# Kernel optimization log

Measured on AMD Instinct MI355X. Metric: run time of the kernel, lower is better.

Reference implementation:

```python
import jax, jax.numpy as jnp
import numpy as np

DELTA = 0.1
PAD = 2  # kernel_size // 2


def _step(x, W):
    # circular padding then VALID 5x5 cross-correlation (matches torch Conv2d circular)
    xp = jnp.pad(x, ((0, 0), (0, 0), (PAD, PAD), (PAD, PAD)), mode='wrap')
    y = jax.lax.conv_general_dilated(
        xp, W, window_strides=(1, 1), padding='VALID',
        dimension_numbers=('NCHW', 'OIHW', 'NCHW'))
    return jnp.clip(x + DELTA * jax.nn.relu(y), 0.0, 1.0)


def setup_inputs() -> dict:
    key = jax.random.key(0)
    k1, k2 = jax.random.split(key)
    x = jax.random.uniform(k1, (16, 3, 1024, 1024), dtype=jnp.float32)
    W = jax.random.normal(k2, (3, 3, 5, 5), dtype=jnp.float32) * 0.2
    return {"x": x, "W": W, "steps": 10}


def reference(x, W, steps):
    for _ in range(steps):
        x = _step(x, W)
    return x
```

## Files before the change

kernel.cpp:

```cpp
#include <hip/hip_runtime.h>


#define HH 1024
#define WW 1024
#define CC 3
#define NB 16
#define KR 2
#define TW 128
#define TH 8
#define LW (TW + 2*KR)
#define LH (TH + 2*KR)
#define DELTA 0.1f

__global__ __launch_bounds__(256)
void ca_step(const float* __restrict__ src, float* __restrict__ dst,
             const float* __restrict__ Wg) {
    __shared__ float tile[CC][LH][LW];
    __shared__ float wsm[CC * 5 * 16];

    const int tid = threadIdx.x;
    const int w0 = blockIdx.x * TW;
    const int h0 = blockIdx.y * TH;
    const int n  = blockIdx.z;

    if (tid < CC * CC * 25) {
        int oc = tid / 75;
        int rem = tid - oc * 75;
        int ic = rem / 25;
        int r2 = rem - ic * 25;
        int kh = r2 / 5;
        int kw = r2 - kh * 5;
        wsm[(ic * 5 + kh) * 16 + oc * 5 + kw] = Wg[tid];
    }

    const float* srcn = src + (size_t)n * CC * HH * WW;
    for (int idx = tid; idx < CC * LH * LW; idx += 256) {
        int c   = idx / (LH * LW);
        int rem = idx - c * (LH * LW);
        int r   = rem / LW;
        int col = rem - r * LW;
        int gh = (h0 + r - KR) & (HH - 1);
        int gw = (w0 + col - KR) & (WW - 1);
        tile[c][r][col] = srcn[((size_t)c * HH + gh) * WW + gw];
    }
    __syncthreads();

    const int tx = tid & 31;
    const int ty = tid >> 5;
    const int xb = tx * 4;

    float acc[CC][4];
#pragma unroll
    for (int oc = 0; oc < CC; ++oc)
#pragma unroll
        for (int j = 0; j < 4; ++j) acc[oc][j] = 0.f;

#pragma unroll
    for (int ic = 0; ic < CC; ++ic) {
#pragma unroll
        for (int kh = 0; kh < 5; ++kh) {
            const float* trow = &tile[ic][ty + kh][xb];
            float v[8];
#pragma unroll
            for (int t = 0; t < 8; ++t) v[t] = trow[t];
            const float* wrow = &wsm[(ic * 5 + kh) * 16];
#pragma unroll
            for (int oc = 0; oc < CC; ++oc) {
#pragma unroll
                for (int kw = 0; kw < 5; ++kw) {
                    const float wv = wrow[oc * 5 + kw];
#pragma unroll
                    for (int j = 0; j < 4; ++j)
                        acc[oc][j] = fmaf(v[kw + j], wv, acc[oc][j]);
                }
            }
        }
    }

    float* dstn = dst + (size_t)n * CC * HH * WW;
    const int h = h0 + ty;
#pragma unroll
    for (int oc = 0; oc < CC; ++oc) {
        float4 o;
        float r0 = fmaxf(acc[oc][0], 0.f);
        float r1 = fmaxf(acc[oc][1], 0.f);
        float r2 = fmaxf(acc[oc][2], 0.f);
        float r3 = fmaxf(acc[oc][3], 0.f);
        o.x = fminf(fmaxf(tile[oc][ty + KR][xb + KR + 0] + DELTA * r0, 0.f), 1.f);
        o.y = fminf(fmaxf(tile[oc][ty + KR][xb + KR + 1] + DELTA * r1, 0.f), 1.f);
        o.z = fminf(fmaxf(tile[oc][ty + KR][xb + KR + 2] + DELTA * r2, 0.f), 1.f);
        o.w = fminf(fmaxf(tile[oc][ty + KR][xb + KR + 3] + DELTA * r3, 0.f), 1.f);
        *(float4*)&dstn[((size_t)oc * HH + h) * WW + w0 + xb] = o;
    }
}

extern "C" void kernel_launch(void* const* d_in, const int* in_sizes, int n_in,
                              void* d_out, int out_size, void* d_ws, size_t ws_size,
                              hipStream_t stream) {
    (void)in_sizes; (void)n_in; (void)out_size;
    const float* x  = (const float*)d_in[0];
    const float* Wg = (const float*)d_in[1];
    const int STEPS = 10;
    float* out = (float*)d_out;
    const size_t buf_bytes = (size_t)NB * CC * HH * WW * sizeof(float);

    dim3 grid(WW / TW, HH / TH, NB);
    dim3 block(256);

    if (ws_size >= buf_bytes) {
        float* tmp = (float*)d_ws;
        const float* s = x;
        for (int i = 1; i <= STEPS; ++i) {
            float* d = (i & 1) ? tmp : out;
            ca_step<<<grid, block, 0, stream>>>(s, d, Wg);
            s = d;
        }
    } else {
        float* tmp = (float*)d_in[0];
        const float* s = x;
        for (int i = 1; i <= STEPS; ++i) {
            float* d = (i & 1) ? out : tmp;
            ca_step<<<grid, block, 0, stream>>>(s, d, Wg);
            s = d;
        }
        hipMemcpyAsync(out, tmp, buf_bytes, hipMemcpyDeviceToDevice, stream);
    }
}
```

Before: 1.740 ms.

## Double tile height, vectorize halo loads and shared reads, reuse weights across two rows

Measured after the change: 1.498 ms. 1.16x faster.

```diff
diff --git a/kernel.cpp b/kernel.cpp
--- a/kernel.cpp
+++ b/kernel.cpp
@@ -5,11 +5,10 @@
 #define WW 1024
 #define CC 3
 #define NB 16
-#define KR 2
 #define TW 128
-#define TH 8
-#define LW (TW + 2*KR)
-#define LH (TH + 2*KR)
+#define TH 16
+#define LW 132
+#define LH 20
 #define DELTA 0.1f
 
 __global__ __launch_bounds__(256)
@@ -22,6 +21,7 @@
     const int w0 = blockIdx.x * TW;
     const int h0 = blockIdx.y * TH;
     const int n  = blockIdx.z;
+    const float* srcn = src + (size_t)n * CC * HH * WW;
 
     if (tid < CC * CC * 25) {
         int oc = tid / 75;
@@ -33,64 +33,97 @@
         wsm[(ic * 5 + kh) * 16 + oc * 5 + kw] = Wg[tid];
     }
 
-    const float* srcn = src + (size_t)n * CC * HH * WW;
-    for (int idx = tid; idx < CC * LH * LW; idx += 256) {
-        int c   = idx / (LH * LW);
-        int rem = idx - c * (LH * LW);
-        int r   = rem / LW;
-        int col = rem - r * LW;
-        int gh = (h0 + r - KR) & (HH - 1);
-        int gw = (w0 + col - KR) & (WW - 1);
-        tile[c][r][col] = srcn[((size_t)c * HH + gh) * WW + gw];
+    for (int f = tid; f < CC * LH * 32; f += 256) {
+        int c   = f / (LH * 32);
+        int rem = f - c * (LH * 32);
+        int row = rem >> 5;
+        int c4  = rem & 31;
+        int gh = (h0 + row - 2) & (HH - 1);
+        const float4 v = *(const float4*)&srcn[((size_t)c * HH + gh) * WW + w0 + 4 * c4];
+        float* t = &tile[c][row][2 + 4 * c4];
+        *(float2*)&t[0] = make_float2(v.x, v.y);
+        *(float2*)&t[2] = make_float2(v.z, v.w);
+    }
+    if (tid < CC * LH * 2) {
+        int side = tid & 1;
+        int rf   = tid >> 1;
+        int c    = rf / LH;
+        int row  = rf - c * LH;
+        int gh = (h0 + row - 2) & (HH - 1);
+        int gw = side ? ((w0 + TW) & (WW - 1)) : ((w0 - 2) & (WW - 1));
+        const float2 v = *(const float2*)&srcn[((size_t)c * HH + gh) * WW + gw];
+        *(float2*)&tile[c][row][side ? (2 + TW) : 0] = v;
     }
     __syncthreads();
 
     const int tx = tid & 31;
     const int ty = tid >> 5;
-    const int xb = tx * 4;
+    const int xb = 4 * tx;
 
-    float acc[CC][4];
+    float acc[2][CC][4];
 #pragma unroll
-    for (int oc = 0; oc < CC; ++oc)
+    for (int rg = 0; rg < 2; ++rg)
 #pragma unroll
-        for (int j = 0; j < 4; ++j) acc[oc][j] = 0.f;
+        for (int oc = 0; oc < CC; ++oc)
+#pragma unroll
+            for (int j = 0; j < 4; ++j) acc[rg][oc][j] = 0.f;
+    float xv[2][CC][4];
 
 #pragma unroll
     for (int ic = 0; ic < CC; ++ic) {
 #pragma unroll
         for (int kh = 0; kh < 5; ++kh) {
-            const float* trow = &tile[ic][ty + kh][xb];
-            float v[8];
+            const float* wrow = &wsm[(ic * 5 + kh) * 16];
+            const float4 wA = *(const float4*)&wrow[0];
+            const float4 wB = *(const float4*)&wrow[4];
+            const float4 wC = *(const float4*)&wrow[8];
+            const float4 wD = *(const float4*)&wrow[12];
+            const float w_[15] = {wA.x, wA.y, wA.z, wA.w,
+                                  wB.x, wB.y, wB.z, wB.w,
+                                  wC.x, wC.y, wC.z, wC.w,
+                                  wD.x, wD.y, wD.z};
+            const float* ra = &tile[ic][ty + kh][xb];
+            const float* rb = &tile[ic][ty + 8 + kh][xb];
+            float va[8], vb[8];
+            *(float4*)&va[0] = *(const float4*)&ra[0];
+            *(float4*)&va[4] = *(const float4*)&ra[4];
+            *(float4*)&vb[0] = *(const float4*)&rb[0];
+            *(float4*)&vb[4] = *(const float4*)&rb[4];
+            if (kh == 2) {
 #pragma unroll
-            for (int t = 0; t < 8; ++t) v[t] = trow[t];
-            const float* wrow = &wsm[(ic * 5 + kh) * 16];
+                for (int j = 0; j < 4; ++j) {
+                    xv[0][ic][j] = va[2 + j];
+                    xv[1][ic][j] = vb[2 + j];
+                }
+            }
 #pragma unroll
             for (int oc = 0; oc < CC; ++oc) {
 #pragma unroll
                 for (int kw = 0; kw < 5; ++kw) {
-                    const float wv = wrow[oc * 5 + kw];
+                    const float wv = w_[oc * 5 + kw];
 #pragma unroll
-                    for (int j = 0; j < 4; ++j)
-                        acc[oc][j] = fmaf(v[kw + j], wv, acc[oc][j]);
+                    for (int j = 0; j < 4; ++j) {
+                        acc[0][oc][j] = fmaf(va[kw + j], wv, acc[0][oc][j]);
+                        acc[1][oc][j] = fmaf(vb[kw + j], wv, acc[1][oc][j]);
+                    }
                 }
             }
         }
     }
 
     float* dstn = dst + (size_t)n * CC * HH * WW;
-    const int h = h0 + ty;
 #pragma unroll
-    for (int oc = 0; oc < CC; ++oc) {
-        float4 o;
-        float r0 = fmaxf(acc[oc][0], 0.f);
-        float r1 = fmaxf(acc[oc][1], 0.f);
-        float r2 = fmaxf(acc[oc][2], 0.f);
-        float r3 = fmaxf(acc[oc][3], 0.f);
-        o.x = fminf(fmaxf(tile[oc][ty + KR][xb + KR + 0] + DELTA * r0, 0.f), 1.f);
-        o.y = fminf(fmaxf(tile[oc][ty + KR][xb + KR + 1] + DELTA * r1, 0.f), 1.f);
-        o.z = fminf(fmaxf(tile[oc][ty + KR][xb + KR + 2] + DELTA * r2, 0.f), 1.f);
-        o.w = fminf(fmaxf(tile[oc][ty + KR][xb + KR + 3] + DELTA * r3, 0.f), 1.f);
-        *(float4*)&dstn[((size_t)oc * HH + h) * WW + w0 + xb] = o;
+    for (int rg = 0; rg < 2; ++rg) {
+        const int h = h0 + ty + rg * 8;
+#pragma unroll
+        for (int oc = 0; oc < CC; ++oc) {
+            float4 o;
+            o.x = fminf(fmaxf(xv[rg][oc][0] + DELTA * fmaxf(acc[rg][oc][0], 0.f), 0.f), 1.f);
+            o.y = fminf(fmaxf(xv[rg][oc][1] + DELTA * fmaxf(acc[rg][oc][1], 0.f), 0.f), 1.f);
+            o.z = fminf(fmaxf(xv[rg][oc][2] + DELTA * fmaxf(acc[rg][oc][2], 0.f), 0.f), 1.f);
+            o.w = fminf(fmaxf(xv[rg][oc][3] + DELTA * fmaxf(acc[rg][oc][3], 0.f), 0.f), 1.f);
+            *(float4*)&dstn[((size_t)oc * HH + h) * WW + w0 + xb] = o;
+        }
     }
 }
 
```
